# Performance work log

Measured on AMD Instinct MI355X. Metric: run time of the kernel, lower is better.

The kernel has to match this reference:

```python
import jax, jax.numpy as jnp
import numpy as np

MUL = 128            # channel multiplicity (node feature channels)
Z = 10               # number of chemical elements (node_attrs dim)
L_DIMS = (1, 3, 5, 7)   # edge SH irrep dims, lmax=3
MM_DIMS = (1, 3)        # magmom SH irrep dims, lmax=1
AVG_NUM_NEIGHBORS = 20.0
N_NODES = 5000
N_EDGES = 100000
R_DIM = 8            # edge radial feature dim
MM_INV_DIM = 8       # magmom invariant feature dim


def _mlp(x, Ws, act):
    # e3nn FullyConnectedNet: variance-preserving linear layers, act between hidden layers
    for W in Ws[:-1]:
        h = x @ W * (1.0 / np.sqrt(W.shape[0]))
        x = act(h) if act is not None else h
    return x @ Ws[-1] * (1.0 / np.sqrt(Ws[-1].shape[0]))


def _conv_tp(x, sh, w, dims):
    # channelwise 'uvu' tensor product: (MUL x 0e) x SH(l) -> MUL x l per l.
    # x:[E,MUL], sh:[E,sum(dims)], w:[E,MUL,n_l]. CG for 0e x l -> l is trivial.
    outs, off = [], 0
    for l, d in enumerate(dims):
        blk = (w[:, :, l] * x)[:, :, None] * sh[:, None, off:off + d]  # [E,MUL,d]
        outs.append(blk.reshape(x.shape[0], MUL * d))
        off += d
    return jnp.concatenate(outs, axis=-1)


def _per_l_linear(x, Ws, dims):
    # e3nn o3.Linear: per-l channel mixing with 1/sqrt(fan_in) normalization
    outs, off = [], 0
    scale = 1.0 / np.sqrt(MUL)
    for l, d in enumerate(dims):
        blk = x[:, off:off + MUL * d].reshape(-1, MUL, d)
        outs.append((jnp.einsum('nud,uv->nvd', blk, Ws[l]) * scale).reshape(-1, MUL * d))
        off += MUL * d
    return jnp.concatenate(outs, axis=-1)


def _skip_tp(x, attrs, Ws, dims):
    # FullyConnectedTensorProduct(irreps_out, Zx0e, irreps_out): per-l bilinear mix
    outs, off = [], 0
    scale = 1.0 / np.sqrt(MUL * attrs.shape[-1])
    for l, d in enumerate(dims):
        blk = x[:, off:off + MUL * d].reshape(-1, MUL, d)
        outs.append((jnp.einsum('nud,nz,uzv->nvd', blk, attrs, Ws[l]) * scale).reshape(-1, MUL * d))
        off += MUL * d
    return jnp.concatenate(outs, axis=-1)


def _reshape_irreps(x, dims):
    # [N, sum(MUL*d)] -> [N, MUL, sum(d)]
    outs, off = [], 0
    for d in dims:
        outs.append(x[:, off:off + MUL * d].reshape(-1, MUL, d))
        off += MUL * d
    return jnp.concatenate(outs, axis=-1)


def setup_inputs() -> dict:
    key = jax.random.key(0)
    ks = jax.random.split(key, 24)
    E, N = N_EDGES, N_NODES
    inp = {
        'node_attrs': jax.random.uniform(ks[0], (N, Z), jnp.float32),
        'node_feats': jax.random.normal(ks[1], (N, MUL), jnp.float32),
        'edge_attrs': jax.random.normal(ks[2], (E, sum(L_DIMS)), jnp.float32),
        'edge_feats': jax.random.uniform(ks[3], (E, R_DIM), jnp.float32),
        'magmom_node_inv_feats': jax.random.normal(ks[4], (N, MM_INV_DIM), jnp.float32),
        'magmom_node_attrs': jax.random.normal(ks[5], (N, sum(MM_DIMS)), jnp.float32),
        'edge_index': jax.random.randint(ks[6], (2, E), 0, N),
    }
    rin = R_DIM + MM_INV_DIM
    inp['W_up'] = jax.random.normal(ks[7], (MUL, MUL), jnp.float32)
    inp['W_rad1'] = jax.random.normal(ks[8], (rin, 64), jnp.float32)
    inp['W_rad2'] = jax.random.normal(ks[9], (64, 64), jnp.float32)
    inp['W_rad3'] = jax.random.normal(ks[10], (64, 64), jnp.float32)
    inp['W_rad4'] = jax.random.normal(ks[11], (64, MUL * len(L_DIMS)), jnp.float32)  # weight_numel=512
    inp['M_rad1'] = jax.random.normal(ks[12], (rin, 64), jnp.float32)
    inp['M_rad2'] = jax.random.normal(ks[13], (64, 64), jnp.float32)
    inp['M_rad3'] = jax.random.normal(ks[14], (64, 64), jnp.float32)
    inp['M_rad4'] = jax.random.normal(ks[15], (64, MUL * len(MM_DIMS)), jnp.float32)  # weight_numel=256
    inp['W_density'] = jax.random.normal(ks[16], (R_DIM, 1), jnp.float32)
    inp['W_lin'] = jax.random.normal(ks[17], (len(L_DIMS), MUL, MUL), jnp.float32)
    inp['W_mlin'] = jax.random.normal(ks[18], (len(MM_DIMS), MUL, MUL), jnp.float32)
    inp['W_skip'] = jax.random.normal(ks[19], (len(L_DIMS), MUL, Z, MUL), jnp.float32)
    inp['W_mskip'] = jax.random.normal(ks[20], (len(L_DIMS), MUL, Z, MUL), jnp.float32)
    return inp


def reference(node_attrs, node_feats, edge_attrs, edge_feats, magmom_node_inv_feats,
              magmom_node_attrs, W_up, W_rad1, W_rad2, W_rad3, W_rad4,
              M_rad1, M_rad2, M_rad3, M_rad4, W_density, W_lin, W_mlin,
              W_skip, W_mskip, edge_index):
    sender, receiver = edge_index[0], edge_index[1]
    E = edge_attrs.shape[0]
    N = node_feats.shape[0]
    silu = jax.nn.silu

    x = node_feats @ W_up * (1.0 / np.sqrt(MUL))  # linear_up
    xj = x[sender]                                # [E, MUL]
    ef_mm = jnp.concatenate([edge_feats, magmom_node_inv_feats[sender]], axis=-1)  # [E, 16]

    tp_w = _mlp(ef_mm, [W_rad1, W_rad2, W_rad3, W_rad4], silu)          # [E, 512]
    edge_density = jnp.tanh((edge_feats @ W_density * (1.0 / np.sqrt(R_DIM))) ** 2)  # [E, 1]

    w4 = tp_w.reshape(E, MUL, len(L_DIMS))
    pre_mji = _conv_tp(xj, edge_attrs, w4, L_DIMS)                      # [E, 2048]

    w_mm = _mlp(ef_mm, [M_rad1, M_rad2, M_rad3, M_rad4], None).reshape(E, MUL, len(MM_DIMS))
    w_mm = w_mm * pre_mji[:, :MUL][:, :, None]                          # density-gated by scalar part
    magmom_mji = _conv_tp(xj, magmom_node_attrs[sender], w_mm, MM_DIMS) # [E, 512]

    w4b = w4 * magmom_mji[:, :MUL][:, :, None]
    mji = _conv_tp(xj, edge_attrs, w4b, L_DIMS)                         # [E, 2048]

    density = jax.ops.segment_sum(edge_density, receiver, num_segments=N)  # [N, 1]
    msg = jax.ops.segment_sum(mji, receiver, num_segments=N)               # [N, 2048]
    mm_msg = jax.ops.segment_sum(magmom_mji, receiver, num_segments=N)     # [N, 512]

    msg = _per_l_linear(msg, W_lin, L_DIMS) / (density + 1.0)
    msg = _skip_tp(msg, node_attrs, W_skip, L_DIMS)

    mm = _per_l_linear(mm_msg, W_mlin, MM_DIMS) / AVG_NUM_NEIGHBORS
    # magmom_linear maps (128x0e+128x1o) -> target irreps: l=2,3 outputs have no path -> zero
    mm = jnp.concatenate([mm, jnp.zeros((N, MUL * (5 + 7)), mm.dtype)], axis=-1)
    mm = _skip_tp(mm, node_attrs, W_mskip, L_DIMS)

    out1 = _reshape_irreps(msg, L_DIMS)  # [N, 128, 16]
    out2 = _reshape_irreps(mm, L_DIMS)   # [N, 128, 16]
    return jnp.stack([out1, out2], axis=0)
```

## Files before the change

kernel.cpp:

```cpp
#include <hip/hip_runtime.h>


__device__ __forceinline__ float silu_f(float x) {
  return x / (1.0f + __expf(-x));
}

__global__ void k_zero_int(int* p, int n) {
  int i = blockIdx.x * blockDim.x + threadIdx.x;
  if (i < n) p[i] = 0;
}

__global__ __launch_bounds__(256) void k_prep(
    const float* __restrict__ M1, const float* __restrict__ M2,
    const float* __restrict__ M3, const float* __restrict__ M4,
    float* __restrict__ Mc) {
  __shared__ float T1[16 * 64];
  __shared__ float T2[16 * 64];
  int t = threadIdx.x;
  for (int i = t; i < 16 * 64; i += 256) {
    int r = i >> 6, c = i & 63;
    float s = 0.f;
    for (int k = 0; k < 64; k++) s += M1[r * 64 + k] * M2[k * 64 + c];
    T1[i] = s;
  }
  __syncthreads();
  for (int i = t; i < 16 * 64; i += 256) {
    int r = i >> 6, c = i & 63;
    float s = 0.f;
    for (int k = 0; k < 64; k++) s += T1[r * 64 + k] * M3[k * 64 + c];
    T2[i] = s;
  }
  __syncthreads();
  for (int i = t; i < 16 * 256; i += 256) {
    int r = i >> 8, c = i & 255;
    float s = 0.f;
    for (int k = 0; k < 64; k++) s += T2[r * 64 + k] * M4[k * 256 + c];
    Mc[i] = s * (1.0f / 2048.0f);
  }
}

__global__ __launch_bounds__(128) void k_up(const float* __restrict__ nf,
                                            const float* __restrict__ W,
                                            float* __restrict__ x, int Nn) {
  int n = blockIdx.x;
  int v = threadIdx.x;
  __shared__ float row[128];
  row[v] = nf[n * 128 + v];
  __syncthreads();
  float s = 0.f;
#pragma unroll 8
  for (int k = 0; k < 128; k++) s += row[k] * W[k * 128 + v];
  x[n * 128 + v] = s * 0.08838834764831845f;
}

__global__ void k_count(const int* __restrict__ recv, int* __restrict__ deg, int E) {
  int e = blockIdx.x * blockDim.x + threadIdx.x;
  if (e < E) atomicAdd(&deg[recv[e]], 1);
}

__global__ __launch_bounds__(1024) void k_scan(const int* __restrict__ deg,
                                               int* __restrict__ rowstart,
                                               int* __restrict__ cursor, int Nn) {
  __shared__ int part[1024];
  int t = threadIdx.x;
  int chunk = (Nn + 1023) / 1024;
  int lo = t * chunk;
  int hi = lo + chunk; if (hi > Nn) hi = Nn; if (lo > Nn) lo = Nn;
  int s = 0;
  for (int i = lo; i < hi; i++) s += deg[i];
  part[t] = s;
  __syncthreads();
  for (int o = 1; o < 1024; o <<= 1) {
    int v = (t >= o) ? part[t - o] : 0;
    __syncthreads();
    part[t] += v;
    __syncthreads();
  }
  int base = (t == 0) ? 0 : part[t - 1];
  for (int i = lo; i < hi; i++) {
    rowstart[i] = base;
    cursor[i] = base;
    base += deg[i];
  }
  if (t == 1023) rowstart[Nn] = part[1023];
}

__global__ void k_fill(const int* __restrict__ recv, int* __restrict__ cursor,
                       int* __restrict__ elist, int E) {
  int e = blockIdx.x * blockDim.x + threadIdx.x;
  if (e < E) {
    int p = atomicAdd(&cursor[recv[e]], 1);
    elist[p] = e;
  }
}

__global__ __launch_bounds__(256) void k_edge(
    const float* __restrict__ edge_feats, const float* __restrict__ mminv,
    const int* __restrict__ sender,
    const float* __restrict__ W1, const float* __restrict__ W2,
    const float* __restrict__ W3, const float* __restrict__ W4,
    const float* __restrict__ Mc, const float* __restrict__ Wd,
    float* __restrict__ w4e, float* __restrict__ wmme, float* __restrict__ dens,
    int E) {
  const int base = blockIdx.x * 8;
  const int t = threadIdx.x;
  __shared__ float ef[8][16];
  __shared__ float hA[8][64];
  __shared__ float hB[8][64];
  const int gwave = t >> 6;
  const int o6 = t & 63;

  if (t < 128) {
    int g = t >> 4, j = t & 15;
    int e = base + g;
    float v = 0.f;
    if (e < E) v = (j < 8) ? edge_feats[e * 8 + j] : mminv[sender[e] * 8 + (j - 8)];
    ef[g][j] = v;
  } else if (t < 136) {
    int g = t - 128;
    int e = base + g;
    if (e < E) {
      float q = 0.f;
#pragma unroll
      for (int k = 0; k < 8; k++) q += edge_feats[e * 8 + k] * Wd[k];
      q *= 0.35355339059327373f;
      dens[e] = tanhf(q * q);
    }
  }
  __syncthreads();

#pragma unroll
  for (int rep = 0; rep < 2; rep++) {
    int g = gwave + rep * 4;
    float s = 0.f;
#pragma unroll
    for (int k = 0; k < 16; k++) s += ef[g][k] * W1[k * 64 + o6];
    hA[g][o6] = silu_f(s * 0.25f);
  }
#pragma unroll
  for (int rep = 0; rep < 2; rep++) {
    int g = gwave + rep * 4;
    float s = 0.f;
#pragma unroll 8
    for (int k = 0; k < 64; k++) s += hA[g][k] * W2[k * 64 + o6];
    hB[g][o6] = silu_f(s * 0.125f);
  }
#pragma unroll
  for (int rep = 0; rep < 2; rep++) {
    int g = gwave + rep * 4;
    float s = 0.f;
#pragma unroll 8
    for (int k = 0; k < 64; k++) s += hB[g][k] * W3[k * 64 + o6];
    hA[g][o6] = silu_f(s * 0.125f);
  }
  __syncthreads();

  float a[8] = {0, 0, 0, 0, 0, 0, 0, 0};
  float b[8] = {0, 0, 0, 0, 0, 0, 0, 0};
#pragma unroll 8
  for (int k = 0; k < 64; k++) {
    float w0 = W4[k * 512 + t];
    float w1 = W4[k * 512 + t + 256];
#pragma unroll
    for (int g = 0; g < 8; g++) {
      float h = hA[g][k];
      a[g] += h * w0;
      b[g] += h * w1;
    }
  }
  float c[8] = {0, 0, 0, 0, 0, 0, 0, 0};
#pragma unroll
  for (int k = 0; k < 16; k++) {
    float w = Mc[k * 256 + t];
#pragma unroll
    for (int g = 0; g < 8; g++) c[g] += ef[g][k] * w;
  }

  const int p0 = (t & 3) * 128 + (t >> 2);
  const int p1 = p0 + 64;
  const int pm = (t & 1) * 128 + (t >> 1);
#pragma unroll
  for (int g = 0; g < 8; g++) {
    int e = base + g;
    if (e < E) {
      w4e[(size_t)e * 512 + p0] = a[g] * 0.125f;
      w4e[(size_t)e * 512 + p1] = b[g] * 0.125f;
      wmme[(size_t)e * 256 + pm] = c[g];
    }
  }
}

__global__ __launch_bounds__(256) void k_edge_hA(
    const float* __restrict__ edge_feats, const float* __restrict__ mminv,
    const int* __restrict__ sender,
    const float* __restrict__ W1, const float* __restrict__ W2,
    const float* __restrict__ W3, const float* __restrict__ Wd,
    float* __restrict__ hAe, float* __restrict__ dens, int E) {
  const int base = blockIdx.x * 8;
  const int t = threadIdx.x;
  __shared__ float ef[8][16];
  __shared__ float hA[8][64];
  __shared__ float hB[8][64];
  const int gwave = t >> 6;
  const int o6 = t & 63;

  if (t < 128) {
    int g = t >> 4, j = t & 15;
    int e = base + g;
    float v = 0.f;
    if (e < E) v = (j < 8) ? edge_feats[e * 8 + j] : mminv[sender[e] * 8 + (j - 8)];
    ef[g][j] = v;
  } else if (t < 136) {
    int g = t - 128;
    int e = base + g;
    if (e < E) {
      float q = 0.f;
#pragma unroll
      for (int k = 0; k < 8; k++) q += edge_feats[e * 8 + k] * Wd[k];
      q *= 0.35355339059327373f;
      dens[e] = tanhf(q * q);
    }
  }
  __syncthreads();

#pragma unroll
  for (int rep = 0; rep < 2; rep++) {
    int g = gwave + rep * 4;
    float s = 0.f;
#pragma unroll
    for (int k = 0; k < 16; k++) s += ef[g][k] * W1[k * 64 + o6];
    hA[g][o6] = silu_f(s * 0.25f);
  }
#pragma unroll
  for (int rep = 0; rep < 2; rep++) {
    int g = gwave + rep * 4;
    float s = 0.f;
#pragma unroll 8
    for (int k = 0; k < 64; k++) s += hA[g][k] * W2[k * 64 + o6];
    hB[g][o6] = silu_f(s * 0.125f);
  }
#pragma unroll
  for (int rep = 0; rep < 2; rep++) {
    int g = gwave + rep * 4;
    float s = 0.f;
#pragma unroll 8
    for (int k = 0; k < 64; k++) s += hB[g][k] * W3[k * 64 + o6];
    int e = base + g;
    if (e < E) hAe[(size_t)e * 64 + o6] = silu_f(s * 0.125f);
  }
}

template <int MODE>
__global__ __launch_bounds__(256) void k_gather_t(
    const float* __restrict__ x, const float* __restrict__ edge_attrs,
    const float* __restrict__ edge_feats, const float* __restrict__ mminv,
    const float* __restrict__ mmattrs, const int* __restrict__ sender,
    const float* __restrict__ W1, const float* __restrict__ W2,
    const float* __restrict__ W3, const float* __restrict__ W4,
    const float* __restrict__ Mc, const float* __restrict__ Wd,
    const float* __restrict__ w4e, const float* __restrict__ wmme,
    const float* __restrict__ dens, const float* __restrict__ hAe,
    const float* __restrict__ Wlin, const float* __restrict__ Wmlin,
    const int* __restrict__ rowstart, const int* __restrict__ elist,
    float* __restrict__ linm, float* __restrict__ linmm, int Nn) {
  const int n = blockIdx.x;
  const int t = threadIdx.x;
  const int start = rowstart[n], end = rowstart[n + 1];

  __shared__ float ef[8][16];
  __shared__ float hA[8][64];
  __shared__ float hB[8][64];
  __shared__ float ubuf[8 * 512 + 8 * 256];
  __shared__ float xjs[8][128];
  __shared__ float shs[8][16];
  __shared__ float mmshs[8][4];
  __shared__ float denss[8];
  __shared__ int eS[8], sS[8];
  __shared__ float dsum_s;

  float (*w4s)[512] = (float (*)[512])ubuf;
  float (*wmms)[256] = (float (*)[256])(ubuf + 8 * 512);
  float (*msg_s)[17] = (float (*)[17])ubuf;
  float (*mm_s)[5] = (float (*)[5])(ubuf + 128 * 17);

  float accm[8] = {0, 0, 0, 0, 0, 0, 0, 0};
  float accmm0 = 0.f, accmm1 = 0.f;
  float accd = 0.f;

  const int u = t & 127;
  const int half = t >> 7;
  const int gwave = t >> 6;
  const int o6 = t & 63;

  for (int base = start; base < end; base += 8) {
    if (t < 8) {
      int g = t;
      if (base + g < end) {
        int e = elist[base + g];
        eS[g] = e;
        sS[g] = sender[e];
        if (MODE < 2) denss[g] = dens[e];
      } else {
        eS[g] = -1;
        sS[g] = 0;
        denss[g] = 0.f;
      }
    }
    __syncthreads();
    int er[8];
    if constexpr (MODE == 0) {
#pragma unroll
      for (int g = 0; g < 8; g++) {
        int ev = eS[g];
        er[g] = ev < 0 ? 0 : ev;
      }
    }
    if (t < 128) {
      int g = t >> 4, j = t & 15;
      int e = eS[g];
      float sh = (e >= 0) ? edge_attrs[e * 16 + j] : 0.f;
      shs[g][j] = sh;
      if constexpr (MODE >= 1) {
        float v = 0.f;
        if (e >= 0) v = (j < 8) ? edge_feats[e * 8 + j] : mminv[sS[g] * 8 + (j - 8)];
        ef[g][j] = v;
      }
    } else if (t < 160) {
      int g = (t - 128) >> 2, j = (t - 128) & 3;
      mmshs[g][j] = (eS[g] >= 0) ? mmattrs[sS[g] * 4 + j] : 0.f;
    }
    for (int i = t; i < 1024; i += 256) {
      int g = i >> 7, uu = i & 127;
      xjs[g][uu] = (eS[g] >= 0) ? x[sS[g] * 128 + uu] : 0.f;
    }
    if constexpr (MODE == 1) {
      for (int i = t; i < 512; i += 256) {
        int g = i >> 6, k = i & 63;
        hA[g][k] = (eS[g] >= 0) ? hAe[(size_t)eS[g] * 64 + k] : 0.f;
      }
    }
    if constexpr (MODE == 2) {
      if (t < 8 && eS[t] >= 0) {
        int e = eS[t];
        float q = 0.f;
#pragma unroll
        for (int k = 0; k < 8; k++) q += edge_feats[e * 8 + k] * Wd[k];
        q *= 0.35355339059327373f;
        denss[t] = tanhf(q * q);
      }
    }
    __syncthreads();

    if constexpr (MODE == 2) {
#pragma unroll
      for (int rep = 0; rep < 2; rep++) {
        int g = gwave + rep * 4;
        float s = 0.f;
#pragma unroll
        for (int k = 0; k < 16; k++) s += ef[g][k] * W1[k * 64 + o6];
        hA[g][o6] = silu_f(s * 0.25f);
      }
#pragma unroll
      for (int rep = 0; rep < 2; rep++) {
        int g = gwave + rep * 4;
        float s = 0.f;
#pragma unroll 8
        for (int k = 0; k < 64; k++) s += hA[g][k] * W2[k * 64 + o6];
        hB[g][o6] = silu_f(s * 0.125f);
      }
#pragma unroll
      for (int rep = 0; rep < 2; rep++) {
        int g = gwave + rep * 4;
        float s = 0.f;
#pragma unroll 8
        for (int k = 0; k < 64; k++) s += hB[g][k] * W3[k * 64 + o6];
        hA[g][o6] = silu_f(s * 0.125f);
      }
      __syncthreads();
    }

    if constexpr (MODE >= 1) {
      {
        float a[8] = {0, 0, 0, 0, 0, 0, 0, 0};
        float b[8] = {0, 0, 0, 0, 0, 0, 0, 0};
#pragma unroll 8
        for (int k = 0; k < 64; k++) {
          float w0 = W4[k * 512 + t];
          float w1 = W4[k * 512 + t + 256];
#pragma unroll
          for (int g = 0; g < 8; g++) {
            float h = hA[g][k];
            a[g] += h * w0;
            b[g] += h * w1;
          }
        }
        int p0 = (t & 3) * 128 + (t >> 2);
        int p1 = (t & 3) * 128 + 64 + (t >> 2);
#pragma unroll
        for (int g = 0; g < 8; g++) {
          w4s[g][p0] = a[g] * 0.125f;
          w4s[g][p1] = b[g] * 0.125f;
        }
      }
      {
        float c[8] = {0, 0, 0, 0, 0, 0, 0, 0};
#pragma unroll
        for (int k = 0; k < 16; k++) {
          float w = Mc[k * 256 + t];
#pragma unroll
          for (int g = 0; g < 8; g++) c[g] += ef[g][k] * w;
        }
        int p = (t & 1) * 128 + (t >> 1);
#pragma unroll
        for (int g = 0; g < 8; g++) wmms[g][p] = c[g];
      }
      __syncthreads();
    }

#pragma unroll 2
    for (int g = 0; g < 8; g++) {
      float w40, w41, w42, w43, wm0, wm1;
      if constexpr (MODE == 0) {
        const size_t b4 = (size_t)er[g] * 512;
        const size_t bm = (size_t)er[g] * 256;
        w40 = w4e[b4 + u];
        w41 = w4e[b4 + 128 + u];
        w42 = w4e[b4 + 256 + u];
        w43 = w4e[b4 + 384 + u];
        wm0 = wmme[bm + u];
        wm1 = wmme[bm + 128 + u];
      } else {
        w40 = w4s[g][u];
        w41 = w4s[g][128 + u];
        w42 = w4s[g][256 + u];
        w43 = w4s[g][384 + u];
        wm0 = wmms[g][u];
        wm1 = wmms[g][128 + u];
      }
      float xj = xjs[g][u];
      float sh0 = shs[g][0];
      float pre0 = w40 * xj * sh0;
      float wg0 = wm0 * pre0;
      float wg1 = wm1 * pre0;
      float mm0 = wg0 * xj * mmshs[g][0];
      float m1 = wg1 * xj;
      float bx = mm0 * xj;
      float b0 = w40 * bx, b1 = w41 * bx, b2 = w42 * bx, b3 = w43 * bx;
      if (half == 0) {
        accmm0 += mm0;
        accmm1 += m1 * mmshs[g][1];
        accm[0] += b0 * sh0;
        accm[1] += b1 * shs[g][1];
        accm[2] += b1 * shs[g][2];
        accm[3] += b1 * shs[g][3];
        accm[4] += b2 * shs[g][4];
        accm[5] += b2 * shs[g][5];
        accm[6] += b2 * shs[g][6];
        accm[7] += b2 * shs[g][7];
      } else {
        accmm0 += m1 * mmshs[g][2];
        accmm1 += m1 * mmshs[g][3];
        accm[0] += b2 * shs[g][8];
        accm[1] += b3 * shs[g][9];
        accm[2] += b3 * shs[g][10];
        accm[3] += b3 * shs[g][11];
        accm[4] += b3 * shs[g][12];
        accm[5] += b3 * shs[g][13];
        accm[6] += b3 * shs[g][14];
        accm[7] += b3 * shs[g][15];
      }
    }
    if (t == 0) {
#pragma unroll
      for (int g = 0; g < 8; g++) accd += denss[g];
    }
  }

  __syncthreads();
#pragma unroll
  for (int j = 0; j < 8; j++) msg_s[u][half * 8 + j] = accm[j];
  mm_s[u][half * 2 + 0] = accmm0;
  mm_s[u][half * 2 + 1] = accmm1;
  if (t == 0) dsum_s = accd;
  __syncthreads();
  const float dinv = 1.0f / (dsum_s + 1.0f);

  float outl[8] = {0, 0, 0, 0, 0, 0, 0, 0};
  if (half == 0) {
    for (int uu = 0; uu < 128; uu++) {
      float wl0 = Wlin[uu * 128 + u];
      float wl1 = Wlin[16384 + uu * 128 + u];
      float wl2 = Wlin[32768 + uu * 128 + u];
      outl[0] += msg_s[uu][0] * wl0;
      outl[1] += msg_s[uu][1] * wl1;
      outl[2] += msg_s[uu][2] * wl1;
      outl[3] += msg_s[uu][3] * wl1;
      outl[4] += msg_s[uu][4] * wl2;
      outl[5] += msg_s[uu][5] * wl2;
      outl[6] += msg_s[uu][6] * wl2;
      outl[7] += msg_s[uu][7] * wl2;
    }
  } else {
    for (int uu = 0; uu < 128; uu++) {
      float wl2 = Wlin[32768 + uu * 128 + u];
      float wl3 = Wlin[49152 + uu * 128 + u];
      outl[0] += msg_s[uu][8] * wl2;
      outl[1] += msg_s[uu][9] * wl3;
      outl[2] += msg_s[uu][10] * wl3;
      outl[3] += msg_s[uu][11] * wl3;
      outl[4] += msg_s[uu][12] * wl3;
      outl[5] += msg_s[uu][13] * wl3;
      outl[6] += msg_s[uu][14] * wl3;
      outl[7] += msg_s[uu][15] * wl3;
    }
  }
  const float scl = 0.08838834764831845f * dinv;
  float4 v0 = make_float4(outl[0] * scl, outl[1] * scl, outl[2] * scl, outl[3] * scl);
  float4 v1 = make_float4(outl[4] * scl, outl[5] * scl, outl[6] * scl, outl[7] * scl);
  float4* lp = (float4*)(linm + (size_t)n * 2048 + u * 16 + half * 8);
  lp[0] = v0;
  lp[1] = v1;

  float om0 = 0.f, om1 = 0.f;
  if (half == 0) {
    for (int uu = 0; uu < 128; uu++) {
      om0 += mm_s[uu][0] * Wmlin[uu * 128 + u];
      om1 += mm_s[uu][1] * Wmlin[16384 + uu * 128 + u];
    }
  } else {
    for (int uu = 0; uu < 128; uu++) {
      float wm1 = Wmlin[16384 + uu * 128 + u];
      om0 += mm_s[uu][2] * wm1;
      om1 += mm_s[uu][3] * wm1;
    }
  }
  const float sm = 0.08838834764831845f / 20.0f;
  *(float2*)(linmm + (size_t)n * 512 + u * 4 + half * 2) = make_float2(om0 * sm, om1 * sm);
}

__global__ void k_zero2(float* __restrict__ out2, int Nn) {
  int i = blockIdx.x * blockDim.x + threadIdx.x;
  if (i < Nn * 128) {
    float4 z = make_float4(0.f, 0.f, 0.f, 0.f);
    float4* p = (float4*)(out2 + (size_t)i * 16);
    p[1] = z;
    p[2] = z;
    p[3] = z;
  }
}

__global__ __launch_bounds__(128) void k_wt(const float* __restrict__ Wskip,
                                            const float* __restrict__ Wmskip,
                                            float* __restrict__ Wt) {
  int bx = blockIdx.x;
  int L = bx >> 7, u = bx & 127;
  int v = threadIdx.x;
  const float* src = (L < 4) ? (Wskip + (size_t)L * 163840)
                             : (Wmskip + (size_t)(L - 4) * 163840);
  float* dst = Wt + (((size_t)L * 128 + u) * 128 + v) * 12;
#pragma unroll
  for (int z = 0; z < 10; z++) dst[z] = src[u * 1280 + z * 128 + v];
  dst[10] = 0.f;
  dst[11] = 0.f;
}

template <int D, int SP>
__device__ __forceinline__ void skip_body2(
    const float* __restrict__ attrs, const float* __restrict__ in, int in_rs,
    int in_us, int in_cb, const float* __restrict__ Wt, float* __restrict__ outp,
    int out_cb, int Nn, int n0, float* lin_s, float (*attrs_s)[10]) {
  const int t = threadIdx.x;
  for (int i = t; i < 160; i += 256) {
    int nn = i / 10, z = i - nn * 10;
    int n = n0 + nn;
    attrs_s[nn][z] = (n < Nn) ? attrs[n * 10 + z] : 0.f;
  }
  for (int i = t; i < 16 * 128 * D; i += 256) {
    int nn = i / (128 * D);
    int r = i - nn * 128 * D;
    int uu = r / D;
    int m = r - uu * D;
    int n = n0 + nn;
    lin_s[(nn * 128 + uu) * SP + m] =
        (n < Nn) ? in[(size_t)n * in_rs + uu * in_us + in_cb + m] : 0.f;
  }
  __syncthreads();

  const int v = t & 127, hf = t >> 7;
  float ar[8][10];
#pragma unroll
  for (int q = 0; q < 8; q++)
#pragma unroll
    for (int z = 0; z < 10; z++) ar[q][z] = attrs_s[hf * 8 + q][z];

  float acc[8][D];
#pragma unroll
  for (int q = 0; q < 8; q++)
#pragma unroll
    for (int m = 0; m < D; m++) acc[q][m] = 0.f;

  const float* wp0 = Wt + (size_t)v * 12;
  for (int u = 0; u < 128; u++) {
    const float* wp = wp0 + (size_t)u * 1536;
    float4 wa = *(const float4*)wp;
    float4 wb = *(const float4*)(wp + 4);
    float2 wc = *(const float2*)(wp + 8);
    float wr[10] = {wa.x, wa.y, wa.z, wa.w, wb.x, wb.y, wb.z, wb.w, wc.x, wc.y};
#pragma unroll
    for (int q = 0; q < 8; q++) {
      float wn = 0.f;
#pragma unroll
      for (int z = 0; z < 10; z++) wn += ar[q][z] * wr[z];
      const float* ls = &lin_s[((hf * 8 + q) * 128 + u) * SP];
#pragma unroll
      for (int m = 0; m < D; m++) acc[q][m] += ls[m] * wn;
    }
  }
#pragma unroll
  for (int q = 0; q < 8; q++) {
    int n = n0 + hf * 8 + q;
    if (n < Nn) {
      float* op = outp + (size_t)n * 2048 + v * 16 + out_cb;
#pragma unroll
      for (int m = 0; m < D; m++) op[m] = acc[q][m] * 0.027950849718747371f;
    }
  }
}

__global__ __launch_bounds__(256) void k_skip(
    const float* __restrict__ attrs, const float* __restrict__ linm,
    const float* __restrict__ linmm, const float* __restrict__ Wt,
    float* __restrict__ out, int Nn) {
  __shared__ float lin_s[16 * 128 * 8];
  __shared__ float attrs_s[16][10];
  const int n0 = blockIdx.x * 16;
  const int job = blockIdx.y;
  const float* Wtj = Wt + (size_t)job * 128 * 128 * 12;
  switch (job) {
    case 0: skip_body2<1, 1>(attrs, linm, 2048, 16, 0, Wtj, out, 0, Nn, n0, lin_s, attrs_s); break;
    case 1: skip_body2<3, 4>(attrs, linm, 2048, 16, 1, Wtj, out, 1, Nn, n0, lin_s, attrs_s); break;
    case 2: skip_body2<5, 8>(attrs, linm, 2048, 16, 4, Wtj, out, 4, Nn, n0, lin_s, attrs_s); break;
    case 3: skip_body2<7, 8>(attrs, linm, 2048, 16, 9, Wtj, out, 9, Nn, n0, lin_s, attrs_s); break;
    case 4: skip_body2<1, 1>(attrs, linmm, 512, 4, 0, Wtj, out + (size_t)Nn * 2048, 0, Nn, n0, lin_s, attrs_s); break;
    case 5: skip_body2<3, 4>(attrs, linmm, 512, 4, 1, Wtj, out + (size_t)Nn * 2048, 1, Nn, n0, lin_s, attrs_s); break;
  }
}

extern "C" void kernel_launch(void* const* d_in, const int* in_sizes, int n_in,
                              void* d_out, int out_size, void* d_ws, size_t ws_size,
                              hipStream_t stream) {
  const float* node_attrs = (const float*)d_in[0];
  const float* node_feats = (const float*)d_in[1];
  const float* edge_attrs = (const float*)d_in[2];
  const float* edge_feats = (const float*)d_in[3];
  const float* mminv = (const float*)d_in[4];
  const float* mmattrs = (const float*)d_in[5];
  const int* edge_index = (const int*)d_in[6];
  const float* W_up = (const float*)d_in[7];
  const float* W1 = (const float*)d_in[8];
  const float* W2 = (const float*)d_in[9];
  const float* W3 = (const float*)d_in[10];
  const float* W4 = (const float*)d_in[11];
  const float* M1 = (const float*)d_in[12];
  const float* M2 = (const float*)d_in[13];
  const float* M3 = (const float*)d_in[14];
  const float* M4 = (const float*)d_in[15];
  const float* Wd = (const float*)d_in[16];
  const float* Wlin = (const float*)d_in[17];
  const float* Wmlin = (const float*)d_in[18];
  const float* Wskip = (const float*)d_in[19];
  const float* Wmskip = (const float*)d_in[20];

  const int N = in_sizes[1] / 128;
  const int E = in_sizes[2] / 16;
  const int* sender = edge_index;
  const int* recv = edge_index + E;

  float* ws = (float*)d_ws;
  float* x = ws;        ws += (size_t)N * 128;
  float* Mc = ws;       ws += 16 * 256;
  float* linm = ws;     ws += (size_t)N * 2048;
  float* linmm = ws;    ws += (size_t)N * 512;
  float* Wt = ws;       ws += (size_t)6 * 128 * 128 * 12;

  const size_t intWords = (size_t)(N + 1) + N + N + E;
  const size_t baseBytes = (size_t)((char*)ws - (char*)d_ws);
  const size_t needA = baseBytes + ((size_t)E * 512 + (size_t)E * 256 + E + intWords) * 4;
  const size_t needB = baseBytes + ((size_t)E * 64 + E + intWords) * 4;
  float* w4e = nullptr; float* wmme = nullptr; float* dens = nullptr; float* hAe = nullptr;
  int mode;
  if (ws_size >= needA) {
    mode = 0;
    w4e = ws;  ws += (size_t)E * 512;
    wmme = ws; ws += (size_t)E * 256;
    dens = ws; ws += E;
  } else if (ws_size >= needB) {
    mode = 1;
    hAe = ws;  ws += (size_t)E * 64;
    dens = ws; ws += E;
  } else {
    mode = 2;
  }
  int* ibuf = (int*)ws;
  int* rowstart = ibuf;
  int* deg = ibuf + (N + 1);
  int* cursor = deg + N;
  int* elist = cursor + N;

  k_zero_int<<<(N + 255) / 256, 256, 0, stream>>>(deg, N);
  k_prep<<<1, 256, 0, stream>>>(M1, M2, M3, M4, Mc);
  k_wt<<<768, 128, 0, stream>>>(Wskip, Wmskip, Wt);
  k_up<<<N, 128, 0, stream>>>(node_feats, W_up, x, N);
  if (mode == 0) {
    k_edge<<<(E + 7) / 8, 256, 0, stream>>>(edge_feats, mminv, sender, W1, W2,
                                            W3, W4, Mc, Wd, w4e, wmme, dens, E);
  } else if (mode == 1) {
    k_edge_hA<<<(E + 7) / 8, 256, 0, stream>>>(edge_feats, mminv, sender, W1,
                                               W2, W3, Wd, hAe, dens, E);
  }
  k_count<<<(E + 255) / 256, 256, 0, stream>>>(recv, deg, E);
  k_scan<<<1, 1024, 0, stream>>>(deg, rowstart, cursor, N);
  k_fill<<<(E + 255) / 256, 256, 0, stream>>>(recv, cursor, elist, E);
  if (mode == 0) {
    k_gather_t<0><<<N, 256, 0, stream>>>(x, edge_attrs, edge_feats, mminv,
                                         mmattrs, sender, W1, W2, W3, W4, Mc,
                                         Wd, w4e, wmme, dens, hAe, Wlin, Wmlin,
                                         rowstart, elist, linm, linmm, N);
  } else if (mode == 1) {
    k_gather_t<1><<<N, 256, 0, stream>>>(x, edge_attrs, edge_feats, mminv,
                                         mmattrs, sender, W1, W2, W3, W4, Mc,
                                         Wd, w4e, wmme, dens, hAe, Wlin, Wmlin,
                                         rowstart, elist, linm, linmm, N);
  } else {
    k_gather_t<2><<<N, 256, 0, stream>>>(x, edge_attrs, edge_feats, mminv,
                                         mmattrs, sender, W1, W2, W3, W4, Mc,
                                         Wd, w4e, wmme, dens, hAe, Wlin, Wmlin,
                                         rowstart, elist, linm, linmm, N);
  }
  k_zero2<<<(N * 128 + 255) / 256, 256, 0, stream>>>((float*)d_out + (size_t)N * 2048, N);
  dim3 gs((N + 15) / 16, 6);
  k_skip<<<gs, 256, 0, stream>>>(node_attrs, linm, linmm, Wt, (float*)d_out, N);
}
```

Before: 967.6 us.

## Split mode-0 gather from per-l linear and double-buffer edge metadata

For the precomputed-weights path, the per-node gather kernel now only accumulates messages, magmom messages and density into global buffers. A separate tiled k_lin kernel then applies the per-l channel mixing with density normalization, processing 16 nodes per block. The gather prefetches the next 8 edges' indices and SH attributes into a double-buffered shared array and loads sender features directly from global, skipping empty edges. This adds global round trips for the message buffers and reuses the w4e region for linm/linmm, which relies on N*2560 fitting inside E*512.

```diff
diff --git a/kernel.cpp b/kernel.cpp
--- a/kernel.cpp
+++ b/kernel.cpp
@@ -1,4 +1,5 @@
 #include <hip/hip_runtime.h>
+#include <stdint.h>
 
 
 __device__ __forceinline__ float silu_f(float x) {
@@ -250,6 +251,198 @@
   }
 }
 
+__global__ __launch_bounds__(256) void k_gather0(
+    const float* __restrict__ x, const float* __restrict__ edge_attrs,
+    const float* __restrict__ mmattrs, const int* __restrict__ sender,
+    const float* __restrict__ w4e, const float* __restrict__ wmme,
+    const float* __restrict__ dens,
+    const int* __restrict__ rowstart, const int* __restrict__ elist,
+    float* __restrict__ msg, float* __restrict__ mmr, float* __restrict__ densN,
+    int Nn) {
+  const int n = blockIdx.x;
+  const int t = threadIdx.x;
+  const int start = rowstart[n], end = rowstart[n + 1];
+
+  __shared__ float shs[2][8][16];
+  __shared__ float mmshs[2][8][4];
+
+  float accm[8] = {0, 0, 0, 0, 0, 0, 0, 0};
+  float accmm0 = 0.f, accmm1 = 0.f, accd = 0.f;
+  const int u = t & 127;
+  const int half = t >> 7;
+
+  int erA[8], srA[8], erB[8], srB[8];
+#pragma unroll
+  for (int g = 0; g < 8; g++) { erA[g] = -1; srA[g] = 0; erB[g] = -1; srB[g] = 0; }
+
+  if (start < end) {
+    int idx = start + (t & 7);
+    int v = (idx < end) ? elist[idx] : -1;
+    int s = (v >= 0) ? sender[v] : 0;
+    float d = (v >= 0) ? dens[v] : 0.f;
+#pragma unroll
+    for (int g = 0; g < 8; g++) {
+      erA[g] = __shfl(v, g);
+      srA[g] = __shfl(s, g);
+      float dg = __shfl(d, g);
+      if (t == 0) accd += dg;
+    }
+    if (t < 128) {
+      int g = t >> 4, j = t & 15;
+      shs[0][g][j] = (erA[g] >= 0) ? edge_attrs[erA[g] * 16 + j] : 0.f;
+    } else if (t < 160) {
+      int g = (t - 128) >> 2, j = (t - 128) & 3;
+      mmshs[0][g][j] = (erA[g] >= 0) ? mmattrs[srA[g] * 4 + j] : 0.f;
+    }
+  }
+  __syncthreads();
+
+  int p = 0;
+  for (int base = start; base < end; base += 8) {
+    const bool hasNext = (base + 8 < end);
+    if (hasNext) {
+      int idx = base + 8 + (t & 7);
+      int v = (idx < end) ? elist[idx] : -1;
+      int s = (v >= 0) ? sender[v] : 0;
+      float d = (v >= 0) ? dens[v] : 0.f;
+#pragma unroll
+      for (int g = 0; g < 8; g++) {
+        erB[g] = __shfl(v, g);
+        srB[g] = __shfl(s, g);
+        float dg = __shfl(d, g);
+        if (t == 0) accd += dg;
+      }
+      if (t < 128) {
+        int g = t >> 4, j = t & 15;
+        shs[p ^ 1][g][j] = (erB[g] >= 0) ? edge_attrs[erB[g] * 16 + j] : 0.f;
+      } else if (t < 160) {
+        int g = (t - 128) >> 2, j = (t - 128) & 3;
+        mmshs[p ^ 1][g][j] = (erB[g] >= 0) ? mmattrs[srB[g] * 4 + j] : 0.f;
+      }
+    }
+#pragma unroll 2
+    for (int g = 0; g < 8; g++) {
+      if (erA[g] < 0) continue;
+      const size_t b4 = (size_t)erA[g] * 512;
+      const size_t bm = (size_t)erA[g] * 256;
+      float w40 = w4e[b4 + u];
+      float w41 = w4e[b4 + 128 + u];
+      float w42 = w4e[b4 + 256 + u];
+      float w43 = w4e[b4 + 384 + u];
+      float wm0 = wmme[bm + u];
+      float wm1 = wmme[bm + 128 + u];
+      float xj = x[(size_t)srA[g] * 128 + u];
+      float sh0 = shs[p][g][0];
+      float pre0 = w40 * xj * sh0;
+      float wg0 = wm0 * pre0;
+      float wg1 = wm1 * pre0;
+      float mm0 = wg0 * xj * mmshs[p][g][0];
+      float m1 = wg1 * xj;
+      float bx = mm0 * xj;
+      float b0 = w40 * bx, b1 = w41 * bx, b2 = w42 * bx, b3 = w43 * bx;
+      if (half == 0) {
+        accmm0 += mm0;
+        accmm1 += m1 * mmshs[p][g][1];
+        accm[0] += b0 * sh0;
+        accm[1] += b1 * shs[p][g][1];
+        accm[2] += b1 * shs[p][g][2];
+        accm[3] += b1 * shs[p][g][3];
+        accm[4] += b2 * shs[p][g][4];
+        accm[5] += b2 * shs[p][g][5];
+        accm[6] += b2 * shs[p][g][6];
+        accm[7] += b2 * shs[p][g][7];
+      } else {
+        accmm0 += m1 * mmshs[p][g][2];
+        accmm1 += m1 * mmshs[p][g][3];
+        accm[0] += b2 * shs[p][g][8];
+        accm[1] += b3 * shs[p][g][9];
+        accm[2] += b3 * shs[p][g][10];
+        accm[3] += b3 * shs[p][g][11];
+        accm[4] += b3 * shs[p][g][12];
+        accm[5] += b3 * shs[p][g][13];
+        accm[6] += b3 * shs[p][g][14];
+        accm[7] += b3 * shs[p][g][15];
+      }
+    }
+    __syncthreads();
+    p ^= 1;
+#pragma unroll
+    for (int g = 0; g < 8; g++) { erA[g] = erB[g]; srA[g] = srB[g]; }
+  }
+
+  float4* mp = (float4*)(msg + (size_t)n * 2048 + u * 16 + half * 8);
+  mp[0] = make_float4(accm[0], accm[1], accm[2], accm[3]);
+  mp[1] = make_float4(accm[4], accm[5], accm[6], accm[7]);
+  *(float2*)(mmr + (size_t)n * 512 + u * 4 + half * 2) = make_float2(accmm0, accmm1);
+  if (t == 0) densN[n] = accd;
+}
+
+template <int D, int SP>
+__device__ __forceinline__ void lin_body(
+    const float* __restrict__ in, int in_rs, int in_us, int in_cb,
+    const float* __restrict__ W, const float* __restrict__ densN, float basescl,
+    bool useDinv, float* __restrict__ outp, int out_rs, int out_us, int out_cb,
+    int Nn, int n0, float* lin_s) {
+  const int t = threadIdx.x;
+  for (int i = t; i < 16 * 128 * D; i += 256) {
+    int nn = i / (128 * D);
+    int r = i - nn * 128 * D;
+    int uu = r / D;
+    int m = r - uu * D;
+    int nd = n0 + nn;
+    lin_s[(nn * 128 + uu) * SP + m] =
+        (nd < Nn) ? in[(size_t)nd * in_rs + uu * in_us + in_cb + m] : 0.f;
+  }
+  __syncthreads();
+
+  const int v = t & 127, hf = t >> 7;
+  float acc[8][D];
+#pragma unroll
+  for (int q = 0; q < 8; q++)
+#pragma unroll
+    for (int m = 0; m < D; m++) acc[q][m] = 0.f;
+
+  for (int uu = 0; uu < 128; uu++) {
+    float wv = W[uu * 128 + v];
+#pragma unroll
+    for (int q = 0; q < 8; q++) {
+      const float* ls = &lin_s[((hf * 8 + q) * 128 + uu) * SP];
+#pragma unroll
+      for (int m = 0; m < D; m++) acc[q][m] += ls[m] * wv;
+    }
+  }
+#pragma unroll
+  for (int q = 0; q < 8; q++) {
+    int nd = n0 + hf * 8 + q;
+    if (nd < Nn) {
+      float scl = basescl;
+      if (useDinv) scl *= 1.0f / (densN[nd] + 1.0f);
+      float* op = outp + (size_t)nd * out_rs + v * out_us + out_cb;
+#pragma unroll
+      for (int m = 0; m < D; m++) op[m] = acc[q][m] * scl;
+    }
+  }
+}
+
+__global__ __launch_bounds__(256) void k_lin(
+    const float* __restrict__ msg, const float* __restrict__ mmr,
+    const float* __restrict__ densN, const float* __restrict__ Wlin,
+    const float* __restrict__ Wmlin, float* __restrict__ linm,
+    float* __restrict__ linmm, int Nn) {
+  __shared__ float lin_s[16 * 128 * 8];
+  const int n0 = blockIdx.x * 16;
+  const float scl = 0.08838834764831845f;
+  const float sm = 0.08838834764831845f / 20.0f;
+  switch (blockIdx.y) {
+    case 0: lin_body<1, 1>(msg, 2048, 16, 0, Wlin, densN, scl, true, linm, 2048, 16, 0, Nn, n0, lin_s); break;
+    case 1: lin_body<3, 4>(msg, 2048, 16, 1, Wlin + 16384, densN, scl, true, linm, 2048, 16, 1, Nn, n0, lin_s); break;
+    case 2: lin_body<5, 8>(msg, 2048, 16, 4, Wlin + 32768, densN, scl, true, linm, 2048, 16, 4, Nn, n0, lin_s); break;
+    case 3: lin_body<7, 8>(msg, 2048, 16, 9, Wlin + 49152, densN, scl, true, linm, 2048, 16, 9, Nn, n0, lin_s); break;
+    case 4: lin_body<1, 1>(mmr, 512, 4, 0, Wmlin, densN, sm, false, linmm, 512, 4, 0, Nn, n0, lin_s); break;
+    case 5: lin_body<3, 4>(mmr, 512, 4, 1, Wmlin + 16384, densN, sm, false, linmm, 512, 4, 1, Nn, n0, lin_s); break;
+  }
+}
+
 template <int MODE>
 __global__ __launch_bounds__(256) void k_gather_t(
     const float* __restrict__ x, const float* __restrict__ edge_attrs,
@@ -258,7 +451,6 @@
     const float* __restrict__ W1, const float* __restrict__ W2,
     const float* __restrict__ W3, const float* __restrict__ W4,
     const float* __restrict__ Mc, const float* __restrict__ Wd,
-    const float* __restrict__ w4e, const float* __restrict__ wmme,
     const float* __restrict__ dens, const float* __restrict__ hAe,
     const float* __restrict__ Wlin, const float* __restrict__ Wmlin,
     const int* __restrict__ rowstart, const int* __restrict__ elist,
@@ -299,7 +491,7 @@
         int e = elist[base + g];
         eS[g] = e;
         sS[g] = sender[e];
-        if (MODE < 2) denss[g] = dens[e];
+        if (MODE == 1) denss[g] = dens[e];
       } else {
         eS[g] = -1;
         sS[g] = 0;
@@ -307,24 +499,13 @@
       }
     }
     __syncthreads();
-    int er[8];
-    if constexpr (MODE == 0) {
-#pragma unroll
-      for (int g = 0; g < 8; g++) {
-        int ev = eS[g];
-        er[g] = ev < 0 ? 0 : ev;
-      }
-    }
     if (t < 128) {
       int g = t >> 4, j = t & 15;
       int e = eS[g];
-      float sh = (e >= 0) ? edge_attrs[e * 16 + j] : 0.f;
-      shs[g][j] = sh;
-      if constexpr (MODE >= 1) {
-        float v = 0.f;
-        if (e >= 0) v = (j < 8) ? edge_feats[e * 8 + j] : mminv[sS[g] * 8 + (j - 8)];
-        ef[g][j] = v;
-      }
+      shs[g][j] = (e >= 0) ? edge_attrs[e * 16 + j] : 0.f;
+      float v = 0.f;
+      if (e >= 0) v = (j < 8) ? edge_feats[e * 8 + j] : mminv[sS[g] * 8 + (j - 8)];
+      ef[g][j] = v;
     } else if (t < 160) {
       int g = (t - 128) >> 2, j = (t - 128) & 3;
       mmshs[g][j] = (eS[g] >= 0) ? mmattrs[sS[g] * 4 + j] : 0.f;
@@ -379,64 +560,50 @@
       __syncthreads();
     }
 
-    if constexpr (MODE >= 1) {
-      {
-        float a[8] = {0, 0, 0, 0, 0, 0, 0, 0};
-        float b[8] = {0, 0, 0, 0, 0, 0, 0, 0};
+    {
+      float a[8] = {0, 0, 0, 0, 0, 0, 0, 0};
+      float b[8] = {0, 0, 0, 0, 0, 0, 0, 0};
 #pragma unroll 8
-        for (int k = 0; k < 64; k++) {
-          float w0 = W4[k * 512 + t];
-          float w1 = W4[k * 512 + t + 256];
-#pragma unroll
-          for (int g = 0; g < 8; g++) {
-            float h = hA[g][k];
-            a[g] += h * w0;
-            b[g] += h * w1;
-          }
+      for (int k = 0; k < 64; k++) {
+        float w0 = W4[k * 512 + t];
+        float w1 = W4[k * 512 + t + 256];
+#pragma unroll
+        for (int g = 0; g < 8; g++) {
+          float h = hA[g][k];
+          a[g] += h * w0;
+          b[g] += h * w1;
         }
-        int p0 = (t & 3) * 128 + (t >> 2);
-        int p1 = (t & 3) * 128 + 64 + (t >> 2);
-#pragma unroll
-        for (int g = 0; g < 8; g++) {
-          w4s[g][p0] = a[g] * 0.125f;
-          w4s[g][p1] = b[g] * 0.125f;
-        }
-      }
-      {
-        float c[8] = {0, 0, 0, 0, 0, 0, 0, 0};
-#pragma unroll
-        for (int k = 0; k < 16; k++) {
-          float w = Mc[k * 256 + t];
-#pragma unroll
-          for (int g = 0; g < 8; g++) c[g] += ef[g][k] * w;
-        }
-        int p = (t & 1) * 128 + (t >> 1);
-#pragma unroll
-        for (int g = 0; g < 8; g++) wmms[g][p] = c[g];
-      }
-      __syncthreads();
-    }
+      }
+      int p0 = (t & 3) * 128 + (t >> 2);
+      int p1 = (t & 3) * 128 + 64 + (t >> 2);
+#pragma unroll
+      for (int g = 0; g < 8; g++) {
+        w4s[g][p0] = a[g] * 0.125f;
+        w4s[g][p1] = b[g] * 0.125f;
+      }
+    }
+    {
+      float c[8] = {0, 0, 0, 0, 0, 0, 0, 0};
+#pragma unroll
+      for (int k = 0; k < 16; k++) {
+        float w = Mc[k * 256 + t];
+#pragma unroll
+        for (int g = 0; g < 8; g++) c[g] += ef[g][k] * w;
+      }
+      int p = (t & 1) * 128 + (t >> 1);
+#pragma unroll
+      for (int g = 0; g < 8; g++) wmms[g][p] = c[g];
+    }
+    __syncthreads();
 
 #pragma unroll 2
     for (int g = 0; g < 8; g++) {
-      float w40, w41, w42, w43, wm0, wm1;
-      if constexpr (MODE == 0) {
-        const size_t b4 = (size_t)er[g] * 512;
-        const size_t bm = (size_t)er[g] * 256;
-        w40 = w4e[b4 + u];
-        w41 = w4e[b4 + 128 + u];
-        w42 = w4e[b4 + 256 + u];
-        w43 = w4e[b4 + 384 + u];
-        wm0 = wmme[bm + u];
-        wm1 = wmme[bm + 128 + u];
-      } else {
-        w40 = w4s[g][u];
-        w41 = w4s[g][128 + u];
-        w42 = w4s[g][256 + u];
-        w43 = w4s[g][384 + u];
-        wm0 = wmms[g][u];
-        wm1 = wmms[g][128 + u];
-      }
+      float w40 = w4s[g][u];
+      float w41 = w4s[g][128 + u];
+      float w42 = w4s[g][256 + u];
+      float w43 = w4s[g][384 + u];
+      float wm0 = wmms[g][u];
+      float wm1 = wmms[g][128 + u];
       float xj = xjs[g][u];
       float sh0 = shs[g][0];
       float pre0 = w40 * xj * sh0;
@@ -677,31 +844,49 @@
   const int* recv = edge_index + E;
 
   float* ws = (float*)d_ws;
-  float* x = ws;        ws += (size_t)N * 128;
-  float* Mc = ws;       ws += 16 * 256;
-  float* linm = ws;     ws += (size_t)N * 2048;
-  float* linmm = ws;    ws += (size_t)N * 512;
-  float* Wt = ws;       ws += (size_t)6 * 128 * 128 * 12;
+  float* x = ws;   ws += (size_t)N * 128;
+  float* Mc = ws;  ws += 16 * 256;
+  float* Wt = ws;  ws += (size_t)6 * 128 * 128 * 12;
 
   const size_t intWords = (size_t)(N + 1) + N + N + E;
-  const size_t baseBytes = (size_t)((char*)ws - (char*)d_ws);
-  const size_t needA = baseBytes + ((size_t)E * 512 + (size_t)E * 256 + E + intWords) * 4;
-  const size_t needB = baseBytes + ((size_t)E * 64 + E + intWords) * 4;
-  float* w4e = nullptr; float* wmme = nullptr; float* dens = nullptr; float* hAe = nullptr;
+  const size_t headBytes = (size_t)((char*)ws - (char*)d_ws);
+  const size_t needA = headBytes +
+      ((size_t)N * 2048 + (size_t)N * 512 + N + intWords +
+       (size_t)E * 512 + (size_t)E * 256 + E) * 4 + 64;
+  const size_t needB = headBytes +
+      ((size_t)N * 2048 + (size_t)N * 512 + (size_t)E * 64 + E + intWords) * 4 + 64;
+
   int mode;
+  float *msg = nullptr, *mmr = nullptr, *densN = nullptr;
+  float *w4e = nullptr, *wmme = nullptr, *dens = nullptr, *hAe = nullptr;
+  float *linm = nullptr, *linmm = nullptr;
+  int* ibuf = nullptr;
+
   if (ws_size >= needA) {
     mode = 0;
-    w4e = ws;  ws += (size_t)E * 512;
-    wmme = ws; ws += (size_t)E * 256;
-    dens = ws; ws += E;
+    msg = ws;   ws += (size_t)N * 2048;
+    mmr = ws;   ws += (size_t)N * 512;
+    densN = ws; ws += N;
+    ibuf = (int*)ws;
+    ws = (float*)(((uintptr_t)(ibuf + intWords) + 15) & ~(uintptr_t)15);
+    w4e = ws;   ws += (size_t)E * 512;
+    wmme = ws;  ws += (size_t)E * 256;
+    dens = ws;  ws += E;
+    linm = w4e;
+    linmm = w4e + (size_t)N * 2048;
   } else if (ws_size >= needB) {
     mode = 1;
-    hAe = ws;  ws += (size_t)E * 64;
-    dens = ws; ws += E;
+    linm = ws;  ws += (size_t)N * 2048;
+    linmm = ws; ws += (size_t)N * 512;
+    hAe = ws;   ws += (size_t)E * 64;
+    dens = ws;  ws += E;
+    ibuf = (int*)ws;
   } else {
     mode = 2;
-  }
-  int* ibuf = (int*)ws;
+    linm = ws;  ws += (size_t)N * 2048;
+    linmm = ws; ws += (size_t)N * 512;
+    ibuf = (int*)ws;
+  }
   int* rowstart = ibuf;
   int* deg = ibuf + (N + 1);
   int* cursor = deg + N;
@@ -721,23 +906,22 @@
   k_count<<<(E + 255) / 256, 256, 0, stream>>>(recv, deg, E);
   k_scan<<<1, 1024, 0, stream>>>(deg, rowstart, cursor, N);
   k_fill<<<(E + 255) / 256, 256, 0, stream>>>(recv, cursor, elist, E);
+  dim3 gs((N + 15) / 16, 6);
   if (mode == 0) {
-    k_gather_t<0><<<N, 256, 0, stream>>>(x, edge_attrs, edge_feats, mminv,
-                                         mmattrs, sender, W1, W2, W3, W4, Mc,
-                                         Wd, w4e, wmme, dens, hAe, Wlin, Wmlin,
-                                         rowstart, elist, linm, linmm, N);
+    k_gather0<<<N, 256, 0, stream>>>(x, edge_attrs, mmattrs, sender, w4e, wmme,
+                                     dens, rowstart, elist, msg, mmr, densN, N);
+    k_lin<<<gs, 256, 0, stream>>>(msg, mmr, densN, Wlin, Wmlin, linm, linmm, N);
   } else if (mode == 1) {
     k_gather_t<1><<<N, 256, 0, stream>>>(x, edge_attrs, edge_feats, mminv,
                                          mmattrs, sender, W1, W2, W3, W4, Mc,
-                                         Wd, w4e, wmme, dens, hAe, Wlin, Wmlin,
-                                         rowstart, elist, linm, linmm, N);
+                                         Wd, dens, hAe, Wlin, Wmlin, rowstart,
+                                         elist, linm, linmm, N);
   } else {
     k_gather_t<2><<<N, 256, 0, stream>>>(x, edge_attrs, edge_feats, mminv,
                                          mmattrs, sender, W1, W2, W3, W4, Mc,
-                                         Wd, w4e, wmme, dens, hAe, Wlin, Wmlin,
-                                         rowstart, elist, linm, linmm, N);
+                                         Wd, dens, hAe, Wlin, Wmlin, rowstart,
+                                         elist, linm, linmm, N);
   }
   k_zero2<<<(N * 128 + 255) / 256, 256, 0, stream>>>((float*)d_out + (size_t)N * 2048, N);
-  dim3 gs((N + 15) / 16, 6);
   k_skip<<<gs, 256, 0, stream>>>(node_attrs, linm, linmm, Wt, (float*)d_out, N);
 }
```

Result: no change. 978.8 us (+1.2%).
